# Optimization experiments

Measured on AMD Instinct MI355X. Metric: run time of the kernel, lower is better.

Reference implementation:

```python
import jax, jax.numpy as jnp
import numpy as np

NQ = 10          # qubits
NT = 32          # tokens (LCU terms)
DM = 512         # d_model
DEG = 2          # qsvt degree
B = 128          # batch
NPQC = 4 * NQ    # params per PQC application
DIM = 2 ** NQ    # statevector dimension


def ansatz14_spec(q, layers=1):
    spec = []
    for _ in range(layers):
        spec += [('ry', (i,)) for i in range(q)]
        spec += [('crx', (i, (i + 1) % q)) for i in range(q - 1, -1, -1)]
        spec += [('ry', (i,)) for i in range(q)]
        spec += [('crx', (i, (i - 1) % q)) for i in [q - 1] + list(range(q - 1))]
    return spec

SPEC = ansatz14_spec(NQ, 1)


def _gate_ry(theta):
    h = theta * 0.5
    c = jnp.cos(h)
    s = jnp.sin(h)
    m = jnp.stack([jnp.stack([c, -s], -1), jnp.stack([s, c], -1)], -2)
    return m.astype(jnp.complex64)  # (N,2,2)


def _gate_rx(theta):
    h = theta * 0.5
    c = jnp.cos(h).astype(jnp.complex64)
    s = (-1j) * jnp.sin(h).astype(jnp.complex64)
    return jnp.stack([jnp.stack([c, s], -1), jnp.stack([s, c], -1)], -2)


def _apply_1q(state, mats, wire, q):
    # state: (N, 2^q) complex; mats: (N,2,2); wire 0 is most significant bit
    N = state.shape[0]
    a = 2 ** wire
    bdim = 2 ** (q - wire - 1)
    s = state.reshape(N, a, 2, bdim)
    return jnp.einsum('nij,najb->naib', mats, s).reshape(N, 2 ** q)


def _apply_crx(state, theta, c, t, q):
    # controlled-RX: control wire c, target wire t
    N = state.shape[0]
    st = state.reshape((N,) + (2,) * q)
    ax = 1 + c
    s0 = jnp.take(st, 0, axis=ax)   # control = 0 branch: untouched
    s1 = jnp.take(st, 1, axis=ax)   # control = 1 branch: apply RX on target
    tp = t if t < c else t - 1      # target wire position after removing control axis
    s1n = _apply_1q(s1.reshape(N, -1), _gate_rx(theta), tp, q - 1).reshape(s1.shape)
    return jnp.stack([s0, s1n], axis=ax).reshape(N, 2 ** q)


def _apply_pqc(state, params, q):
    # params: (N, NPQC); fixed small gate list -> Python loop is fine
    for k, (fn, w) in enumerate(SPEC):
        th = params[:, k]
        if fn == 'ry':
            state = _apply_1q(state, _gate_ry(th), w[0], q)
        else:
            state = _apply_crx(state, th, w[0], w[1], q)
    return state


def _apply_lcu(states, params, lcu):
    # states: (B, DIM) complex; params: (B, L, NPQC); lcu: (B, L) complex
    Bn, L = lcu.shape
    rep = jnp.repeat(states, L, axis=0)                    # (B*L, DIM)
    st = _apply_pqc(rep, params.reshape(Bn * L, NPQC), NQ)
    return jnp.einsum('bld,bl->bd', st.reshape(Bn, L, DIM), lcu)


def _measure_xyz(state, q):
    # Pauli expectations per wire: order [X_0..X_{q-1}, Y_0.., Z_0..]
    N = state.shape[0]
    xs, ys, zs = [], [], []
    for w in range(q):
        s = state.reshape(N, 2 ** w, 2, -1)
        a0, a1 = s[:, :, 0, :], s[:, :, 1, :]
        cross = jnp.sum(jnp.conj(a0) * a1, axis=(1, 2))
        xs.append(2.0 * jnp.real(cross))
        ys.append(2.0 * jnp.imag(cross))
        zs.append(jnp.sum(jnp.abs(a0) ** 2 - jnp.abs(a1) ** 2, axis=(1, 2)))
    return jnp.stack(xs + ys + zs, axis=1).astype(jnp.float32)  # (B, 3q)


def reference(tokens_emb, W, b, lcu_re, lcu_im, qsvt_coeffs, ff_params):
    Bn, L, D = tokens_emb.shape
    L = min(L, NT)
    pqc_params = tokens_emb[:, :L] @ W.T + b               # (B, L, NPQC)
    lcu = (lcu_re + 1j * lcu_im).astype(jnp.complex64)[:L]
    lcu = lcu / jnp.sum(jnp.abs(lcu))
    lcu_b = jnp.broadcast_to(lcu[None], (Bn, L))
    init = jnp.zeros((Bn, DIM), jnp.complex64).at[:, 0].set(1.0)
    acc = qsvt_coeffs[0].astype(jnp.complex64) * init
    mono = init
    for k in range(1, DEG + 1):
        mono = _apply_lcu(mono, pqc_params, lcu_b)
        acc = acc + qsvt_coeffs[k].astype(jnp.complex64) * mono
    state = acc / jnp.sum(jnp.abs(qsvt_coeffs))
    state = state / jnp.linalg.norm(state, axis=-1, keepdims=True)
    ffp = jnp.broadcast_to(ff_params[None], (Bn, NPQC))
    state = _apply_pqc(state, ffp, NQ)
    return _measure_xyz(state, NQ)


def setup_inputs():
    key = jax.random.key(0)
    ks = jax.random.split(key, 7)
    return {
        'tokens_emb': jax.random.normal(ks[0], (B, NT, DM), jnp.float32),
        'W': jax.random.normal(ks[1], (NPQC, DM), jnp.float32) * 0.05,
        'b': jax.random.normal(ks[2], (NPQC,), jnp.float32),
        'lcu_re': jax.random.normal(ks[3], (NT,), jnp.float32),
        'lcu_im': jax.random.normal(ks[4], (NT,), jnp.float32),
        'qsvt_coeffs': jax.random.normal(ks[5], (DEG + 1,), jnp.float32),
        'ff_params': jax.random.normal(ks[6], (NPQC,), jnp.float32),
    }
```

## Files before the change

kernel.cpp:

```cpp
#include <hip/hip_runtime.h>
#include <hip/hip_bf16.h>


#define NQ   10
#define NT   32
#define DM   512
#define BATCH 128
#define NPQC 40
#define DIM  1024
#define NROWS (BATCH * NT)
#define PSTRIDE (BATCH * DIM)

typedef float v2f __attribute__((ext_vector_type(2)));

__device__ __forceinline__ v2f Jrot(v2f v) {
  return __builtin_shufflevector(v, -v, 1, 2);
}
__device__ __forceinline__ v2f Jc(v2f v) {
  return __builtin_shufflevector(-v, v, 1, 2);
}


template<int B>
__device__ __forceinline__ void g_ry(v2f (&a)[16], float c, float s) {
  static_assert(B >= 6, "RY targets must be register bits");
  constexpr int m = 1 << (B - 6);
#pragma unroll
  for (int r = 0; r < 16; ++r) {
    if (!(r & m)) {
      int r1 = r | m;
      v2f a0 = a[r], a1 = a[r1];
      a[r]  = c * a0 - s * a1;
      a[r1] = s * a0 + c * a1;
    }
  }
}

template<int BC, int BT>
__device__ __forceinline__ void g_crx(v2f (&a)[16], int lane, float c, float s) {
  static_assert(BT >= 6, "CRX targets must be register bits");
  constexpr int m = 1 << (BT - 6);
  bool lane_ok = (BC >= 6) || ((lane >> BC) & 1);
  float ce = lane_ok ? c : 1.f;
  float se = lane_ok ? s : 0.f;
#pragma unroll
  for (int r = 0; r < 16; ++r) {
    if (!(r & m)) {
      if constexpr (BC >= 6) { if (!((r >> (BC - 6)) & 1)) continue; }
      int r1 = r | m;
      v2f a0 = a[r], a1 = a[r1];
      a[r]  = ce * a0 + se * Jrot(a1);
      a[r1] = ce * a1 + se * Jrot(a0);
    }
  }
}

template<int L0, int L1, int L2, int L3>
__device__ __forceinline__ void remap(v2f (&a)[16], v2f* __restrict__ slab,
                                      int lane) {
  constexpr int LM = (1 << L0) | (1 << L1) | (1 << L2) | (1 << L3);
#pragma unroll
  for (int r = 0; r < 16; ++r) {
    int f = 0;
    if (L0 < 4 && (r & 1)) f |= 1 << L0;
    if (L1 < 4 && (r & 2)) f |= 1 << L1;
    if (L2 < 4 && (r & 4)) f |= 1 << L2;
    if (L3 < 4 && (r & 8)) f |= 1 << L3;
    slab[r * 64 + (lane ^ f)] = a[r];
  }
  asm volatile("s_waitcnt lgkmcnt(0)" ::: "memory");
  int la = lane & ~LM & 63;
  la |= ((lane >> L0) & 1) << 6;
  la |= ((lane >> L1) & 1) << 7;
  la |= ((lane >> L2) & 1) << 8;
  la |= ((lane >> L3) & 1) << 9;
  if (L0 < 4) la |= ((lane >> L0) & 1) << L0;
  if (L1 < 4) la |= ((lane >> L1) & 1) << L1;
  if (L2 < 4) la |= ((lane >> L2) & 1) << L2;
  if (L3 < 4) la |= ((lane >> L3) & 1) << L3;
#pragma unroll
  for (int r = 0; r < 16; ++r) {
    int rc = ((r & 1) ? (1 << L0) : 0) | ((r & 2) ? (1 << L1) : 0)
           | ((r & 4) ? (1 << L2) : 0) | ((r & 8) ? (1 << L3) : 0);
    a[r] = slab[la ^ rc];
  }
}

template<bool SKIP_HEAD>
__device__ __forceinline__ void apply_pqc_phased(v2f (&a)[16],
    const float2* __restrict__ cs, v2f* __restrict__ slab, int lane) {
#define RYt(B, t)      g_ry<B>(a, t.x, t.y);
#define CXt(BC, BT, t) g_crx<BC, BT>(a, lane, t.x, t.y);
  float2 t10 = cs[10], t11 = cs[11], t12 = cs[12];
  if constexpr (!SKIP_HEAD) {
    float2 t0 = cs[0], t1 = cs[1], t2 = cs[2], t3 = cs[3];
    float2 t4 = cs[4], t5 = cs[5], t6 = cs[6], t7 = cs[7];
    float2 t8 = cs[8], t9 = cs[9];
    RYt(9,t0) RYt(8,t1) RYt(7,t2) RYt(6,t3)
    remap<5,4,3,2>(a, slab, lane);
    RYt(6,t4) RYt(7,t5) RYt(8,t6) RYt(9,t7)
    remap<1,0,2,3>(a, slab, lane);
    RYt(6,t8) RYt(7,t9)
  }
  CXt(7,8,t10) CXt(6,7,t11) CXt(3,6,t12)
  float2 t13 = cs[13], t14 = cs[14], t15 = cs[15], t16 = cs[16];
  remap<1,0,2,3>(a, slab, lane);
  CXt(8,9,t13) CXt(7,8,t14) CXt(6,7,t15) CXt(5,6,t16)
  float2 t17 = cs[17], t18 = cs[18], t19 = cs[19];
  float2 t20 = cs[20], t21 = cs[21], t22 = cs[22], t23 = cs[23];
  remap<2,3,4,5>(a, slab, lane);
  CXt(8,9,t17) CXt(7,8,t18) CXt(6,7,t19)
  RYt(6,t20) RYt(7,t21) RYt(8,t22) RYt(9,t23)
  float2 t24 = cs[24], t25 = cs[25], t26 = cs[26], t27 = cs[27];
  remap<2,3,4,5>(a, slab, lane);
  RYt(6,t24) RYt(7,t25) RYt(8,t26) RYt(9,t27)
  float2 t28 = cs[28], t29 = cs[29];
  float2 t30 = cs[30], t31 = cs[31], t32 = cs[32], t33 = cs[33];
  remap<1,0,2,3>(a, slab, lane);
  RYt(6,t28) RYt(7,t29)
  CXt(7,6,t30) CXt(8,7,t31) CXt(9,8,t32) CXt(4,9,t33)
  float2 t34 = cs[34], t35 = cs[35], t36 = cs[36], t37 = cs[37];
  remap<4,5,1,0>(a, slab, lane);
  CXt(7,6,t34) CXt(8,7,t35) CXt(9,8,t36) CXt(2,9,t37)
  float2 t38 = cs[38], t39 = cs[39];
  remap<2,3,4,5>(a, slab, lane);
  CXt(7,6,t38) CXt(8,7,t39)
#undef RYt
#undef CXt
}

__device__ __forceinline__ int p8_lane_canon(int lane) {
  return (((lane >> 1) & 1) << 9) | ((lane & 1) << 8) | (((lane >> 2) & 1) << 7)
       | (((lane >> 3) & 1) << 6) | (((lane >> 4) & 1) << 5) | (((lane >> 5) & 1) << 4);
}

__global__ __launch_bounds__(256) void params_kernel(
    const float* __restrict__ emb, const float* __restrict__ W,
    const float* __restrict__ bias,
    const float* __restrict__ lcu_re, const float* __restrict__ lcu_im,
    const float* __restrict__ ffp,
    float2* __restrict__ cs, float2* __restrict__ ffcs, float2* __restrict__ lcu) {
  int blk = blockIdx.x;
  int tid = threadIdx.x;
  if (blk == 256) {
    if (tid < NPQC) {
      float h = 0.5f * ffp[tid];
      ffcs[tid] = make_float2(cosf(h), sinf(h));
    }
    if (tid == 64) {
      float ssum = 0.f;
      for (int i = 0; i < NT; ++i) {
        float re = lcu_re[i], im = lcu_im[i];
        ssum += sqrtf(re * re + im * im);
      }
      float inv = 1.f / ssum;
      for (int i = 0; i < NT; ++i)
        lcu[i] = make_float2(lcu_re[i] * inv, lcu_im[i] * inv);
    }
    return;
  }

  __shared__ float Asl[16 * 516];
  int row0 = blk * 16;

  const float4* eg = (const float4*)(emb + (size_t)row0 * DM);
#pragma unroll
  for (int i = 0; i < 8; ++i) {
    int e = tid + i * 256;
    int r = e >> 7, k4 = e & 127;
    float4 v = eg[e];
    *(float4*)&Asl[r * 516 + k4 * 4] = v;
  }
  __syncthreads();

  int kq = tid >> 6;
  int lane = tid & 63;
  int rg = lane >> 3;
  int cg = lane & 7;

  const float* Ar0 = &Asl[(2 * rg) * 516 + kq * 128];
  const float* Ar1 = Ar0 + 516;
  const float* Bg  = W + (size_t)(5 * cg) * DM + kq * 128;

  float acc[2][5] = {};
#pragma unroll 4
  for (int k = 0; k < 128; k += 4) {
    float4 a0 = *(const float4*)(Ar0 + k);
    float4 a1 = *(const float4*)(Ar1 + k);
#pragma unroll
    for (int j = 0; j < 5; ++j) {
      float4 b = *(const float4*)(Bg + j * DM + k);
      acc[0][j] += a0.x * b.x + a0.y * b.y + a0.z * b.z + a0.w * b.w;
      acc[1][j] += a1.x * b.x + a1.y * b.y + a1.z * b.z + a1.w * b.w;
    }
  }

  __syncthreads();
  float* red = Asl;
#pragma unroll
  for (int i = 0; i < 2; ++i)
#pragma unroll
    for (int j = 0; j < 5; ++j)
      red[kq * 644 + (2 * rg + i) * 40 + 5 * cg + j] = acc[i][j];
  __syncthreads();

  for (int o = tid; o < 640; o += 256) {
    float v = bias[o % 40] + red[o] + red[644 + o] + red[1288 + o] + red[1932 + o];
    float h = 0.5f * v;
    cs[(size_t)blk * 640 + o] = make_float2(cosf(h), sinf(h));
  }
}

template<bool FIRST>
__global__ __launch_bounds__(256) void pqc_step(
    const float2* __restrict__ cs, const float2* __restrict__ lcu,
    const v2f* __restrict__ src, v2f* __restrict__ dst) {
  __shared__ v2f slabs[4][1024];
  int lane = threadIdx.x & 63;
  int wvu = __builtin_amdgcn_readfirstlane(threadIdx.x >> 6);
  int blk = blockIdx.x;
  int b = blk >> 3, qq = blk & 7;
  int l = qq * 4 + wvu;
  const float2* csrow = cs + (size_t)(b * NT + l) * NPQC;
  v2f* slab = slabs[wvu];

  v2f a[16];
  if constexpr (FIRST) {
    float2 f5 = csrow[5], f4 = csrow[4], f6 = csrow[6], f7 = csrow[7];
    float2 f2 = csrow[2], f3 = csrow[3];
    float2 f8 = csrow[8], f9 = csrow[9], f0 = csrow[0], f1 = csrow[1];
    float lp = ((lane & 1) ? f5.y : f5.x);
    lp *= ((lane & 2) ? f4.y : f4.x);
    lp *= ((lane & 4) ? f6.y : f6.x);
    lp *= ((lane & 8) ? f7.y : f7.x);
    lp *= ((lane & 16) ? f2.y : f2.x);
    lp *= ((lane & 32) ? f3.y : f3.x);
#pragma unroll
    for (int r = 0; r < 16; ++r) {
      float rp = ((r & 1) ? f8.y : f8.x) * ((r & 2) ? f9.y : f9.x)
               * ((r & 4) ? f0.y : f0.x) * ((r & 8) ? f1.y : f1.x);
      a[r].x = lp * rp;
      a[r].y = 0.f;
    }
  } else {
    const v2f* s = src + (size_t)b * DIM;
#pragma unroll
    for (int r = 0; r < 16; ++r) {
      int n = r * 64 + lane;
      v2f acc = (v2f)(0.f);
#pragma unroll
      for (int q = 0; q < 8; ++q) acc += s[n + q * PSTRIDE];
      a[r] = acc;
    }
  }

  apply_pqc_phased<FIRST>(a, csrow, slab, lane);

  float2 w = lcu[l];
  int pl = p8_lane_canon(lane);
  pl ^= (pl >> 5);
#pragma unroll
  for (int r = 0; r < 16; ++r) {
    int rc = ((r & 1) << 3) | ((r & 2) << 1) | ((r & 4) >> 1) | ((r & 8) >> 3);
    slab[pl ^ rc] = w.x * a[r] + w.y * Jc(a[r]);
  }
  __syncthreads();

  v2f* dst_b = dst + (size_t)(qq * BATCH + b) * DIM;
#pragma unroll
  for (int i = 0; i < 4; ++i) {
    int n = threadIdx.x + i * 256;
    int ph = n ^ (n >> 5);
    v2f sum = (v2f)(0.f);
#pragma unroll
    for (int s = 0; s < 4; ++s) sum += slabs[s][ph];
    dst_b[n] = sum;
  }
}

__global__ __launch_bounds__(256) void final_kernel(
    const v2f* __restrict__ part1, const v2f* __restrict__ part2,
    const float* __restrict__ qsvt, const float2* __restrict__ ffcs,
    float* __restrict__ out) {
  __shared__ v2f slabs[4][1024];
  int lane = threadIdx.x & 63;
  int wvu = __builtin_amdgcn_readfirstlane(threadIdx.x >> 6);
  int b = blockIdx.x * 4 + wvu;
  float q0 = qsvt[0], q1 = qsvt[1], q2 = qsvt[2];

  v2f a[16];
  const v2f* p1 = part1 + (size_t)b * DIM;
  const v2f* p2 = part2 + (size_t)b * DIM;
#pragma unroll
  for (int r = 0; r < 16; ++r) {
    int n = r * 64 + lane;
    v2f m1 = (v2f)(0.f), m2 = (v2f)(0.f);
#pragma unroll
    for (int q = 0; q < 8; ++q) {
      m1 += p1[n + q * PSTRIDE];
      m2 += p2[n + q * PSTRIDE];
    }
    a[r] = q1 * m1 + q2 * m2;
  }
  if (lane == 0) a[0].x += q0;

  float nn = 0.f;
#pragma unroll
  for (int r = 0; r < 16; ++r) nn += a[r].x * a[r].x + a[r].y * a[r].y;
#pragma unroll
  for (int o = 1; o < 64; o <<= 1) nn += __shfl_xor(nn, o);
  float inv = 1.f / sqrtf(nn);
#pragma unroll
  for (int r = 0; r < 16; ++r) a[r] *= inv;

  apply_pqc_phased<false>(a, ffcs, slabs[wvu], lane);

  constexpr int BPOS[10] = {1, 0, 2, 3, 4, 5, 6, 7, 8, 9};
#pragma unroll
  for (int w = 0; w < NQ; ++w) {
    const int p = BPOS[w];
    float xr = 0.f, xi = 0.f, zz = 0.f;
    if (p >= 6) {
      const int m = 1 << (p - 6);
#pragma unroll
      for (int r = 0; r < 16; ++r) {
        float mag = a[r].x * a[r].x + a[r].y * a[r].y;
        zz += (r & m) ? -mag : mag;
        if (!(r & m)) {
          int r1 = r | m;
          xr += a[r].x * a[r1].x + a[r].y * a[r1].y;
          xi += a[r].x * a[r1].y - a[r].y * a[r1].x;
        }
      }
    } else {
      const int lm = 1 << p;
      bool lo = !(lane & lm);
#pragma unroll
      for (int r = 0; r < 16; ++r) {
        float mag = a[r].x * a[r].x + a[r].y * a[r].y;
        zz += lo ? mag : -mag;
        float pr = __shfl_xor(a[r].x, lm);
        float pi = __shfl_xor(a[r].y, lm);
        if (lo) {
          xr += a[r].x * pr + a[r].y * pi;
          xi += a[r].x * pi - a[r].y * pr;
        }
      }
    }
#pragma unroll
    for (int o = 1; o < 64; o <<= 1) {
      xr += __shfl_xor(xr, o);
      xi += __shfl_xor(xi, o);
      zz += __shfl_xor(zz, o);
    }
    if (lane == 0) {
      out[b * 30 + w]      = 2.f * xr;
      out[b * 30 + 10 + w] = 2.f * xi;
      out[b * 30 + 20 + w] = zz;
    }
  }
}


extern "C" void kernel_launch(void* const* d_in, const int* in_sizes, int n_in,
                              void* d_out, int out_size, void* d_ws, size_t ws_size,
                              hipStream_t stream) {
  const float* emb    = (const float*)d_in[0];
  const float* W      = (const float*)d_in[1];
  const float* bias   = (const float*)d_in[2];
  const float* lcu_re = (const float*)d_in[3];
  const float* lcu_im = (const float*)d_in[4];
  const float* qsvt   = (const float*)d_in[5];
  const float* ffp    = (const float*)d_in[6];
  float* out = (float*)d_out;

  char* ws = (char*)d_ws;
  float2* cs    = (float2*)ws;
  float2* ffcs  = (float2*)(ws + 1310720);
  float2* lcu   = (float2*)(ws + 1311040);
  v2f*    part1 = (v2f*)(ws + 1311744);
  v2f*    part2 = (v2f*)(ws + 1311744 + 8388608);

  params_kernel<<<257, 256, 0, stream>>>(emb, W, bias, lcu_re, lcu_im, ffp,
                                         cs, ffcs, lcu);
  pqc_step<true><<<1024, 256, 0, stream>>>(cs, lcu, nullptr, part1);
  pqc_step<false><<<1024, 256, 0, stream>>>(cs, lcu, part1, part2);
  final_kernel<<<BATCH / 4, 256, 0, stream>>>(part1, part2, qsvt, ffcs, out);
}
```

Before: 154.4 us.

## Process two LCU terms per wavefront with packed dual-state LDS remaps

```diff
diff --git a/kernel.cpp b/kernel.cpp
--- a/kernel.cpp
+++ b/kernel.cpp
@@ -12,6 +12,7 @@
 #define PSTRIDE (BATCH * DIM)
 
 typedef float v2f __attribute__((ext_vector_type(2)));
+typedef float v4f __attribute__((ext_vector_type(4)));
 
 __device__ __forceinline__ v2f Jrot(v2f v) {
   return __builtin_shufflevector(v, -v, 1, 2);
@@ -86,22 +87,54 @@
   }
 }
 
-template<bool SKIP_HEAD>
+template<int L0, int L1, int L2, int L3>
+__device__ __forceinline__ void remap2(v2f (&a)[16], v2f (&b)[16],
+                                       v4f* __restrict__ slab, int lane) {
+  constexpr int LM = (1 << L0) | (1 << L1) | (1 << L2) | (1 << L3);
+#pragma unroll
+  for (int r = 0; r < 16; ++r) {
+    int f = 0;
+    if (L0 < 4 && (r & 1)) f |= 1 << L0;
+    if (L1 < 4 && (r & 2)) f |= 1 << L1;
+    if (L2 < 4 && (r & 4)) f |= 1 << L2;
+    if (L3 < 4 && (r & 8)) f |= 1 << L3;
+    v4f pk;
+    pk.x = a[r].x; pk.y = a[r].y; pk.z = b[r].x; pk.w = b[r].y;
+    slab[r * 64 + (lane ^ f)] = pk;
+  }
+  asm volatile("s_waitcnt lgkmcnt(0)" ::: "memory");
+  int la = lane & ~LM & 63;
+  la |= ((lane >> L0) & 1) << 6;
+  la |= ((lane >> L1) & 1) << 7;
+  la |= ((lane >> L2) & 1) << 8;
+  la |= ((lane >> L3) & 1) << 9;
+  if (L0 < 4) la |= ((lane >> L0) & 1) << L0;
+  if (L1 < 4) la |= ((lane >> L1) & 1) << L1;
+  if (L2 < 4) la |= ((lane >> L2) & 1) << L2;
+  if (L3 < 4) la |= ((lane >> L3) & 1) << L3;
+#pragma unroll
+  for (int r = 0; r < 16; ++r) {
+    int rc = ((r & 1) ? (1 << L0) : 0) | ((r & 2) ? (1 << L1) : 0)
+           | ((r & 4) ? (1 << L2) : 0) | ((r & 8) ? (1 << L3) : 0);
+    v4f v = slab[la ^ rc];
+    a[r].x = v.x; a[r].y = v.y;
+    b[r].x = v.z; b[r].y = v.w;
+  }
+}
+
 __device__ __forceinline__ void apply_pqc_phased(v2f (&a)[16],
     const float2* __restrict__ cs, v2f* __restrict__ slab, int lane) {
 #define RYt(B, t)      g_ry<B>(a, t.x, t.y);
 #define CXt(BC, BT, t) g_crx<BC, BT>(a, lane, t.x, t.y);
   float2 t10 = cs[10], t11 = cs[11], t12 = cs[12];
-  if constexpr (!SKIP_HEAD) {
-    float2 t0 = cs[0], t1 = cs[1], t2 = cs[2], t3 = cs[3];
-    float2 t4 = cs[4], t5 = cs[5], t6 = cs[6], t7 = cs[7];
-    float2 t8 = cs[8], t9 = cs[9];
-    RYt(9,t0) RYt(8,t1) RYt(7,t2) RYt(6,t3)
-    remap<5,4,3,2>(a, slab, lane);
-    RYt(6,t4) RYt(7,t5) RYt(8,t6) RYt(9,t7)
-    remap<1,0,2,3>(a, slab, lane);
-    RYt(6,t8) RYt(7,t9)
-  }
+  float2 t0 = cs[0], t1 = cs[1], t2 = cs[2], t3 = cs[3];
+  float2 t4 = cs[4], t5 = cs[5], t6 = cs[6], t7 = cs[7];
+  float2 t8 = cs[8], t9 = cs[9];
+  RYt(9,t0) RYt(8,t1) RYt(7,t2) RYt(6,t3)
+  remap<5,4,3,2>(a, slab, lane);
+  RYt(6,t4) RYt(7,t5) RYt(8,t6) RYt(9,t7)
+  remap<1,0,2,3>(a, slab, lane);
+  RYt(6,t8) RYt(7,t9)
   CXt(7,8,t10) CXt(6,7,t11) CXt(3,6,t12)
   float2 t13 = cs[13], t14 = cs[14], t15 = cs[15], t16 = cs[16];
   remap<1,0,2,3>(a, slab, lane);
@@ -129,9 +162,83 @@
 #undef CXt
 }
 
+template<bool SKIP_HEAD>
+__device__ __forceinline__ void apply_pqc2(v2f (&A)[16], v2f (&B)[16],
+    const float2* __restrict__ pA, const float2* __restrict__ pB,
+    v4f* __restrict__ slab, int lane) {
+#define RY2(B_, u, v)      g_ry<B_>(A, u.x, u.y); g_ry<B_>(B, v.x, v.y);
+#define CX2(BC, BT, u, v)  g_crx<BC,BT>(A, lane, u.x, u.y); g_crx<BC,BT>(B, lane, v.x, v.y);
+  float2 uA10 = pA[10], uA11 = pA[11], uA12 = pA[12];
+  float2 uB10 = pB[10], uB11 = pB[11], uB12 = pB[12];
+  if constexpr (!SKIP_HEAD) {
+    float2 a0=pA[0],a1=pA[1],a2=pA[2],a3=pA[3],a4=pA[4];
+    float2 a5=pA[5],a6=pA[6],a7=pA[7],a8=pA[8],a9=pA[9];
+    float2 b0=pB[0],b1=pB[1],b2=pB[2],b3=pB[3],b4=pB[4];
+    float2 b5=pB[5],b6=pB[6],b7=pB[7],b8=pB[8],b9=pB[9];
+    RY2(9,a0,b0) RY2(8,a1,b1) RY2(7,a2,b2) RY2(6,a3,b3)
+    remap2<5,4,3,2>(A, B, slab, lane);
+    RY2(6,a4,b4) RY2(7,a5,b5) RY2(8,a6,b6) RY2(9,a7,b7)
+    remap2<1,0,2,3>(A, B, slab, lane);
+    RY2(6,a8,b8) RY2(7,a9,b9)
+  }
+  CX2(7,8,uA10,uB10) CX2(6,7,uA11,uB11) CX2(3,6,uA12,uB12)
+  float2 uA13=pA[13],uA14=pA[14],uA15=pA[15],uA16=pA[16];
+  float2 uB13=pB[13],uB14=pB[14],uB15=pB[15],uB16=pB[16];
+  remap2<1,0,2,3>(A, B, slab, lane);
+  CX2(8,9,uA13,uB13) CX2(7,8,uA14,uB14) CX2(6,7,uA15,uB15) CX2(5,6,uA16,uB16)
+  float2 uA17=pA[17],uA18=pA[18],uA19=pA[19];
+  float2 uB17=pB[17],uB18=pB[18],uB19=pB[19];
+  float2 uA20=pA[20],uA21=pA[21],uA22=pA[22],uA23=pA[23];
+  float2 uB20=pB[20],uB21=pB[21],uB22=pB[22],uB23=pB[23];
+  remap2<2,3,4,5>(A, B, slab, lane);
+  CX2(8,9,uA17,uB17) CX2(7,8,uA18,uB18) CX2(6,7,uA19,uB19)
+  RY2(6,uA20,uB20) RY2(7,uA21,uB21) RY2(8,uA22,uB22) RY2(9,uA23,uB23)
+  float2 uA24=pA[24],uA25=pA[25],uA26=pA[26],uA27=pA[27];
+  float2 uB24=pB[24],uB25=pB[25],uB26=pB[26],uB27=pB[27];
+  remap2<2,3,4,5>(A, B, slab, lane);
+  RY2(6,uA24,uB24) RY2(7,uA25,uB25) RY2(8,uA26,uB26) RY2(9,uA27,uB27)
+  float2 uA28=pA[28],uA29=pA[29];
+  float2 uB28=pB[28],uB29=pB[29];
+  float2 uA30=pA[30],uA31=pA[31],uA32=pA[32],uA33=pA[33];
+  float2 uB30=pB[30],uB31=pB[31],uB32=pB[32],uB33=pB[33];
+  remap2<1,0,2,3>(A, B, slab, lane);
+  RY2(6,uA28,uB28) RY2(7,uA29,uB29)
+  CX2(7,6,uA30,uB30) CX2(8,7,uA31,uB31) CX2(9,8,uA32,uB32) CX2(4,9,uA33,uB33)
+  float2 uA34=pA[34],uA35=pA[35],uA36=pA[36],uA37=pA[37];
+  float2 uB34=pB[34],uB35=pB[35],uB36=pB[36],uB37=pB[37];
+  remap2<4,5,1,0>(A, B, slab, lane);
+  CX2(7,6,uA34,uB34) CX2(8,7,uA35,uB35) CX2(9,8,uA36,uB36) CX2(2,9,uA37,uB37)
+  float2 uA38=pA[38],uA39=pA[39];
+  float2 uB38=pB[38],uB39=pB[39];
+  remap2<2,3,4,5>(A, B, slab, lane);
+  CX2(7,6,uA38,uB38) CX2(8,7,uA39,uB39)
+#undef RY2
+#undef CX2
+}
+
 __device__ __forceinline__ int p8_lane_canon(int lane) {
   return (((lane >> 1) & 1) << 9) | ((lane & 1) << 8) | (((lane >> 2) & 1) << 7)
        | (((lane >> 3) & 1) << 6) | (((lane >> 4) & 1) << 5) | (((lane >> 5) & 1) << 4);
+}
+
+__device__ __forceinline__ void product_init(v2f (&a)[16],
+    const float2* __restrict__ csrow, int lane) {
+  float2 f5 = csrow[5], f4 = csrow[4], f6 = csrow[6], f7 = csrow[7];
+  float2 f2 = csrow[2], f3 = csrow[3];
+  float2 f8 = csrow[8], f9 = csrow[9], f0 = csrow[0], f1 = csrow[1];
+  float lp = ((lane & 1) ? f5.y : f5.x);
+  lp *= ((lane & 2) ? f4.y : f4.x);
+  lp *= ((lane & 4) ? f6.y : f6.x);
+  lp *= ((lane & 8) ? f7.y : f7.x);
+  lp *= ((lane & 16) ? f2.y : f2.x);
+  lp *= ((lane & 32) ? f3.y : f3.x);
+#pragma unroll
+  for (int r = 0; r < 16; ++r) {
+    float rp = ((r & 1) ? f8.y : f8.x) * ((r & 2) ? f9.y : f9.x)
+             * ((r & 4) ? f0.y : f0.x) * ((r & 8) ? f1.y : f1.x);
+    a[r].x = lp * rp;
+    a[r].y = 0.f;
+  }
 }
 
 __global__ __launch_bounds__(256) void params_kernel(
@@ -212,36 +319,23 @@
 }
 
 template<bool FIRST>
-__global__ __launch_bounds__(256) void pqc_step(
+__global__ __launch_bounds__(128, 2) void pqc_step(
     const float2* __restrict__ cs, const float2* __restrict__ lcu,
     const v2f* __restrict__ src, v2f* __restrict__ dst) {
-  __shared__ v2f slabs[4][1024];
+  __shared__ v4f slabs[2][1024];
   int lane = threadIdx.x & 63;
   int wvu = __builtin_amdgcn_readfirstlane(threadIdx.x >> 6);
   int blk = blockIdx.x;
   int b = blk >> 3, qq = blk & 7;
-  int l = qq * 4 + wvu;
-  const float2* csrow = cs + (size_t)(b * NT + l) * NPQC;
-  v2f* slab = slabs[wvu];
-
-  v2f a[16];
+  int l0 = qq * 4 + 2 * wvu;
+  const float2* csA = cs + (size_t)(b * NT + l0) * NPQC;
+  const float2* csB = csA + NPQC;
+  v4f* slab = slabs[wvu];
+
+  v2f A[16], Bs[16];
   if constexpr (FIRST) {
-    float2 f5 = csrow[5], f4 = csrow[4], f6 = csrow[6], f7 = csrow[7];
-    float2 f2 = csrow[2], f3 = csrow[3];
-    float2 f8 = csrow[8], f9 = csrow[9], f0 = csrow[0], f1 = csrow[1];
-    float lp = ((lane & 1) ? f5.y : f5.x);
-    lp *= ((lane & 2) ? f4.y : f4.x);
-    lp *= ((lane & 4) ? f6.y : f6.x);
-    lp *= ((lane & 8) ? f7.y : f7.x);
-    lp *= ((lane & 16) ? f2.y : f2.x);
-    lp *= ((lane & 32) ? f3.y : f3.x);
-#pragma unroll
-    for (int r = 0; r < 16; ++r) {
-      float rp = ((r & 1) ? f8.y : f8.x) * ((r & 2) ? f9.y : f9.x)
-               * ((r & 4) ? f0.y : f0.x) * ((r & 8) ? f1.y : f1.x);
-      a[r].x = lp * rp;
-      a[r].y = 0.f;
-    }
+    product_init(A, csA, lane);
+    product_init(Bs, csB, lane);
   } else {
     const v2f* s = src + (size_t)b * DIM;
 #pragma unroll
@@ -250,35 +344,37 @@
       v2f acc = (v2f)(0.f);
 #pragma unroll
       for (int q = 0; q < 8; ++q) acc += s[n + q * PSTRIDE];
-      a[r] = acc;
-    }
-  }
-
-  apply_pqc_phased<FIRST>(a, csrow, slab, lane);
-
-  float2 w = lcu[l];
+      A[r] = acc;
+      Bs[r] = acc;
+    }
+  }
+
+  apply_pqc2<FIRST>(A, Bs, csA, csB, slab, lane);
+
+  float2 wA = lcu[l0], wB = lcu[l0 + 1];
+  v2f* slab2 = (v2f*)slabs[wvu];
   int pl = p8_lane_canon(lane);
   pl ^= (pl >> 5);
 #pragma unroll
   for (int r = 0; r < 16; ++r) {
     int rc = ((r & 1) << 3) | ((r & 2) << 1) | ((r & 4) >> 1) | ((r & 8) >> 3);
-    slab[pl ^ rc] = w.x * a[r] + w.y * Jc(a[r]);
+    slab2[pl ^ rc] = wA.x * A[r] + wA.y * Jc(A[r])
+                   + wB.x * Bs[r] + wB.y * Jc(Bs[r]);
   }
   __syncthreads();
 
+  v2f* s0 = (v2f*)slabs[0];
+  v2f* s1 = (v2f*)slabs[1];
   v2f* dst_b = dst + (size_t)(qq * BATCH + b) * DIM;
 #pragma unroll
-  for (int i = 0; i < 4; ++i) {
-    int n = threadIdx.x + i * 256;
+  for (int i = 0; i < 8; ++i) {
+    int n = threadIdx.x + i * 128;
     int ph = n ^ (n >> 5);
-    v2f sum = (v2f)(0.f);
-#pragma unroll
-    for (int s = 0; s < 4; ++s) sum += slabs[s][ph];
-    dst_b[n] = sum;
-  }
-}
-
-__global__ __launch_bounds__(256) void final_kernel(
+    dst_b[n] = s0[ph] + s1[ph];
+  }
+}
+
+__global__ __launch_bounds__(256, 2) void final_kernel(
     const v2f* __restrict__ part1, const v2f* __restrict__ part2,
     const float* __restrict__ qsvt, const float2* __restrict__ ffcs,
     float* __restrict__ out) {
@@ -313,9 +409,10 @@
 #pragma unroll
   for (int r = 0; r < 16; ++r) a[r] *= inv;
 
-  apply_pqc_phased<false>(a, ffcs, slabs[wvu], lane);
+  apply_pqc_phased(a, ffcs, slabs[wvu], lane);
 
   constexpr int BPOS[10] = {1, 0, 2, 3, 4, 5, 6, 7, 8, 9};
+  float prt[30];
 #pragma unroll
   for (int w = 0; w < NQ; ++w) {
     const int p = BPOS[w];
@@ -347,17 +444,21 @@
         }
       }
     }
-#pragma unroll
-    for (int o = 1; o < 64; o <<= 1) {
-      xr += __shfl_xor(xr, o);
-      xi += __shfl_xor(xi, o);
-      zz += __shfl_xor(zz, o);
-    }
-    if (lane == 0) {
-      out[b * 30 + w]      = 2.f * xr;
-      out[b * 30 + 10 + w] = 2.f * xi;
-      out[b * 30 + 20 + w] = zz;
-    }
+    prt[w]      = xr;
+    prt[10 + w] = xi;
+    prt[20 + w] = zz;
+  }
+
+  float* tb = (float*)slabs[wvu];
+#pragma unroll
+  for (int v = 0; v < 30; ++v) tb[v * 65 + lane] = prt[v];
+  asm volatile("s_waitcnt lgkmcnt(0)" ::: "memory");
+  if (lane < 30) {
+    float s = 0.f;
+#pragma unroll
+    for (int k = 0; k < 64; ++k) s += tb[lane * 65 + k];
+    float sc = (lane < 20) ? 2.f : 1.f;
+    out[b * 30 + lane] = sc * s;
   }
 }
 
@@ -383,7 +484,7 @@
 
   params_kernel<<<257, 256, 0, stream>>>(emb, W, bias, lcu_re, lcu_im, ffp,
                                          cs, ffcs, lcu);
-  pqc_step<true><<<1024, 256, 0, stream>>>(cs, lcu, nullptr, part1);
-  pqc_step<false><<<1024, 256, 0, stream>>>(cs, lcu, part1, part2);
+  pqc_step<true><<<1024, 128, 0, stream>>>(cs, lcu, nullptr, part1);
+  pqc_step<false><<<1024, 128, 0, stream>>>(cs, lcu, part1, part2);
   final_kernel<<<BATCH / 4, 256, 0, stream>>>(part1, part2, qsvt, ffcs, out);
 }
```

Measured after the change: 159.3 us. +3.1%, slower.
